# Optimization experiments

Measured on AMD Instinct MI355X. Metric: run time of the kernel, lower is better.

## Reference

```python
import jax, jax.numpy as jnp
import numpy as np

D = 1024
K = 3  # depthwise conv kernel size, causal (left pad K-1)


def setup_inputs() -> dict:
    key = jax.random.key(0)
    ks = jax.random.split(key, 6)
    B, L = 16, 2048
    x = jax.random.normal(ks[0], (B, L, D), dtype=jnp.float32)
    s_in = 1.0 / np.sqrt(D)
    Win = jax.random.uniform(ks[1], (3 * D, D), minval=-s_in, maxval=s_in, dtype=jnp.float32)
    bin_ = jax.random.uniform(ks[2], (3 * D,), minval=-s_in, maxval=s_in, dtype=jnp.float32)
    # depthwise Conv1d weight (D, 1, K) -> stored as (D, K)
    s_c = 1.0 / np.sqrt(K)  # fan_in = in_channels/groups * K = K
    wconv = jax.random.uniform(ks[3], (D, K), minval=-s_c, maxval=s_c, dtype=jnp.float32)
    Wout = jax.random.uniform(ks[4], (D, D), minval=-s_in, maxval=s_in, dtype=jnp.float32)
    bout = jax.random.uniform(ks[5], (D,), minval=-s_in, maxval=s_in, dtype=jnp.float32)
    return {"x": x, "Win": Win, "bin_": bin_, "wconv": wconv, "Wout": Wout, "bout": bout}


def reference(x, Win, bin_, wconv, Wout, bout):
    # x: (B, L, D). in_proj -> (B, L, 3D); chunk along channel dim == last dim here
    BCx = jnp.einsum('bld,ed->ble', x, Win) + bin_
    Bg, Cg, xg = jnp.split(BCx, 3, axis=-1)  # each (B, L, D)
    Bx = Bg * xg
    L = Bx.shape[1]
    # causal depthwise conv: pad K-1 zeros on the left of time axis
    xp = jnp.pad(Bx, ((0, 0), (K - 1, 0), (0, 0)))
    conv_out = (wconv[:, 0] * xp[:, 0:L]
                + wconv[:, 1] * xp[:, 1:L + 1]
                + wconv[:, 2] * xp[:, 2:L + 2])  # (B, L, D)
    y = Cg * conv_out
    return jnp.einsum('bld,ed->ble', y, Wout) + bout
```

## Files before the change

### kernel.cpp

```cpp
#include <hip/hip_runtime.h>
#include <hip/hip_bf16.h>

#define D_    1024
#define LSEQ  2048
#define BATCH 16
#define M_    (BATCH * LSEQ)
#define K_    1024
#define N1    3072

typedef __bf16 bf16x8 __attribute__((ext_vector_type(8)));
typedef float  f32x4  __attribute__((ext_vector_type(4)));
typedef unsigned short us8 __attribute__((ext_vector_type(8)));

__device__ __forceinline__ unsigned short f2bf(float f) {
  unsigned u = __float_as_uint(f);
  u += 0x7FFFu + ((u >> 16) & 1u);
  return (unsigned short)(u >> 16);
}

__device__ __forceinline__ float bf2f(unsigned short h) {
  return __uint_as_float(((unsigned)h) << 16);
}

__global__ __launch_bounds__(256) void cvt_f32_bf16(const float* __restrict__ in,
                                                    unsigned short* __restrict__ out,
                                                    int n4) {
  int i = blockIdx.x * 256 + threadIdx.x;
  if (i < n4) {
    float4 v = ((const float4*)in)[i];
    ushort4 o;
    o.x = f2bf(v.x); o.y = f2bf(v.y); o.z = f2bf(v.z); o.w = f2bf(v.w);
    ((ushort4*)out)[i] = o;
  }
}

#define BM 128
#define BN 128
#define BK 32

__device__ __forceinline__ void gload_lds16(const void* g, void* l) {
  __builtin_amdgcn_global_load_lds((const __attribute__((address_space(1))) void*)g,
                                   (__attribute__((address_space(3))) void*)l,
                                   16, 0, 0);
}

template <int OUT_BF16>
__global__ __launch_bounds__(256) void gemm_bt(const unsigned short* __restrict__ A,
                                               const unsigned short* __restrict__ B,
                                               const float* __restrict__ bias,
                                               void* __restrict__ Cv,
                                               int M, int N, int K) {
  __shared__ unsigned short As[BM * BK];
  __shared__ unsigned short Bs[BN * BK];

  const int tid  = threadIdx.x;
  const int lane = tid & 63;
  const int wave = tid >> 6;
  const int quad = lane >> 4;
  const int l16  = lane & 15;
  const int wm   = wave & 1;
  const int wn   = wave >> 1;
  const int m0   = blockIdx.y * BM;
  const int n0   = blockIdx.x * BN;

  const int r0 = tid >> 2;
  const int s0 = (tid & 3) * 8;
  const unsigned short* a0 = A + (long)(m0 + r0) * K + s0;
  const unsigned short* a1 = a0 + (long)64 * K;
  const unsigned short* b0 = B + (long)(n0 + r0) * K + s0;
  const unsigned short* b1 = b0 + (long)64 * K;
  unsigned short* lA0 = &As[tid * 8];
  unsigned short* lA1 = &As[(256 + tid) * 8];
  unsigned short* lB0 = &Bs[tid * 8];
  unsigned short* lB1 = &Bs[(256 + tid) * 8];

  f32x4 acc[4][4] = {};

  for (int k0 = 0; k0 < K; k0 += BK) {
    gload_lds16(a0 + k0, lA0);
    gload_lds16(a1 + k0, lA1);
    gload_lds16(b0 + k0, lB0);
    gload_lds16(b1 + k0, lB1);
    __syncthreads();

    bf16x8 af[4], bfr[4];
#pragma unroll
    for (int mi = 0; mi < 4; ++mi)
      af[mi] = *(const bf16x8*)&As[(wm * 64 + mi * 16 + l16) * BK + quad * 8];
#pragma unroll
    for (int ni = 0; ni < 4; ++ni)
      bfr[ni] = *(const bf16x8*)&Bs[(wn * 64 + ni * 16 + l16) * BK + quad * 8];

#pragma unroll
    for (int mi = 0; mi < 4; ++mi)
#pragma unroll
      for (int ni = 0; ni < 4; ++ni)
        acc[mi][ni] = __builtin_amdgcn_mfma_f32_16x16x32_bf16(af[mi], bfr[ni],
                                                              acc[mi][ni], 0, 0, 0);
    __syncthreads();
  }

#pragma unroll
  for (int ni = 0; ni < 4; ++ni) {
    int col = n0 + wn * 64 + ni * 16 + l16;
    float bv = bias[col];
#pragma unroll
    for (int mi = 0; mi < 4; ++mi) {
      int row = m0 + wm * 64 + mi * 16 + quad * 4;
      f32x4 v = acc[mi][ni];
#pragma unroll
      for (int r = 0; r < 4; ++r) {
        float o = v[r] + bv;
        if (OUT_BF16)
          ((unsigned short*)Cv)[(long)(row + r) * N + col] = f2bf(o);
        else
          ((float*)Cv)[(long)(row + r) * N + col] = o;
      }
    }
  }
}

__global__ __launch_bounds__(256) void conv_mul(const unsigned short* __restrict__ BCx,
                                                const float* __restrict__ wconv,
                                                unsigned short* __restrict__ y) {
  __shared__ float wt[3][D_];
  for (int i = threadIdx.x; i < D_; i += 256) {
    wt[0][i] = wconv[i * 3 + 0];
    wt[1][i] = wconv[i * 3 + 1];
    wt[2][i] = wconv[i * 3 + 2];
  }
  __syncthreads();

  int idx = blockIdx.x * 256 + threadIdx.x;
  int bl  = idx >> 7;
  int d8  = (idx & 127) * 8;
  int l   = bl & (LSEQ - 1);
  const unsigned short* row = BCx + (long)bl * N1;

  us8 bg0 = *(const us8*)&row[d8];
  us8 xg0 = *(const us8*)&row[2048 + d8];
  us8 cg  = *(const us8*)&row[1024 + d8];

  float bx0[8], bx1[8], bx2[8];
#pragma unroll
  for (int j = 0; j < 8; ++j) { bx0[j] = bf2f(bg0[j]) * bf2f(xg0[j]); bx1[j] = 0.f; bx2[j] = 0.f; }

  if (l >= 1) {
    us8 bg1 = *(const us8*)&row[-N1 + d8];
    us8 xg1 = *(const us8*)&row[-N1 + 2048 + d8];
#pragma unroll
    for (int j = 0; j < 8; ++j) bx1[j] = bf2f(bg1[j]) * bf2f(xg1[j]);
  }
  if (l >= 2) {
    us8 bg2 = *(const us8*)&row[-2 * N1 + d8];
    us8 xg2 = *(const us8*)&row[-2 * N1 + 2048 + d8];
#pragma unroll
    for (int j = 0; j < 8; ++j) bx2[j] = bf2f(bg2[j]) * bf2f(xg2[j]);
  }

  us8 outv;
#pragma unroll
  for (int j = 0; j < 8; ++j) {
    float conv = wt[0][d8 + j] * bx2[j] + wt[1][d8 + j] * bx1[j] + wt[2][d8 + j] * bx0[j];
    outv[j] = f2bf(bf2f(cg[j]) * conv);
  }
  *(us8*)&y[(long)bl * D_ + d8] = outv;
}

extern "C" void kernel_launch(void* const* d_in, const int* in_sizes, int n_in,
                              void* d_out, int out_size, void* d_ws, size_t ws_size,
                              hipStream_t stream) {
  const float* x     = (const float*)d_in[0];
  const float* Win   = (const float*)d_in[1];
  const float* bin   = (const float*)d_in[2];
  const float* wconv = (const float*)d_in[3];
  const float* Wout  = (const float*)d_in[4];
  const float* bout  = (const float*)d_in[5];

  char* ws = (char*)d_ws;
  unsigned short* x_b    = (unsigned short*)(ws);
  unsigned short* Win_b  = (unsigned short*)(ws + 67108864);
  unsigned short* Wout_b = (unsigned short*)(ws + 73400320);
  unsigned short* BCx_b  = (unsigned short*)(ws + 75497472);
  unsigned short* y_b    = (unsigned short*)(ws + 276824064);

  cvt_f32_bf16<<<(M_ * K_ / 4) / 256, 256, 0, stream>>>(x, x_b, M_ * K_ / 4);
  cvt_f32_bf16<<<(N1 * K_ / 4) / 256, 256, 0, stream>>>(Win, Win_b, N1 * K_ / 4);
  cvt_f32_bf16<<<(D_ * K_ / 4) / 256, 256, 0, stream>>>(Wout, Wout_b, D_ * K_ / 4);

  {
    dim3 grid(N1 / BN, M_ / BM);
    gemm_bt<1><<<grid, 256, 0, stream>>>(x_b, Win_b, bin, BCx_b, M_, N1, K_);
  }

  conv_mul<<<(M_ * (D_ / 8)) / 256, 256, 0, stream>>>(BCx_b, wconv, y_b);

  {
    dim3 grid(D_ / BN, M_ / BM);
    gemm_bt<0><<<grid, 256, 0, stream>>>(y_b, Wout_b, bout, d_out, M_, D_, K_);
  }
}
```

Baseline: 668.1 us.

## Fuse gating and causal conv into GEMM epilogues, drop BCx intermediate

Splits the in-projection GEMM into two launches. The first computes the B and x gate columns together and writes only their product Bx in bf16. The second computes the C gate columns and applies the causal depthwise conv over Bx plus the C multiply in its epilogue, which removes the standalone conv kernel and the 3D-wide BCx buffer. Epilogues now stage tiles through LDS for coalesced vector stores, at the cost of extra barriers and LDS reuse.

Measured after the change: 631.4 us. 5.5% less time.

```diff
diff --git a/kernel.cpp b/kernel.cpp
--- a/kernel.cpp
+++ b/kernel.cpp
@@ -3,21 +3,17 @@
 
 #define D_    1024
 #define LSEQ  2048
-#define BATCH 16
-#define M_    (BATCH * LSEQ)
+#define M_    32768
 #define K_    1024
-#define N1    3072
 
 typedef __bf16 bf16x8 __attribute__((ext_vector_type(8)));
 typedef float  f32x4  __attribute__((ext_vector_type(4)));
-typedef unsigned short us8 __attribute__((ext_vector_type(8)));
 
 __device__ __forceinline__ unsigned short f2bf(float f) {
   unsigned u = __float_as_uint(f);
   u += 0x7FFFu + ((u >> 16) & 1u);
   return (unsigned short)(u >> 16);
 }
-
 __device__ __forceinline__ float bf2f(unsigned short h) {
   return __uint_as_float(((unsigned)h) << 16);
 }
@@ -34,8 +30,6 @@
   }
 }
 
-#define BM 128
-#define BN 128
 #define BK 32
 
 __device__ __forceinline__ void gload_lds16(const void* g, void* l) {
@@ -44,14 +38,18 @@
                                    16, 0, 0);
 }
 
-template <int OUT_BF16>
-__global__ __launch_bounds__(256) void gemm_bt(const unsigned short* __restrict__ A,
-                                               const unsigned short* __restrict__ B,
-                                               const float* __restrict__ bias,
-                                               void* __restrict__ Cv,
-                                               int M, int N, int K) {
-  __shared__ unsigned short As[BM * BK];
-  __shared__ unsigned short Bs[BN * BK];
+template <int MODE>
+__global__ __launch_bounds__(256) void gemm_fused(const unsigned short* __restrict__ A,
+                                                  const unsigned short* __restrict__ Wb,
+                                                  const float* __restrict__ biasA,
+                                                  const float* __restrict__ biasB,
+                                                  const unsigned short* __restrict__ Bx,
+                                                  const float* __restrict__ wconv,
+                                                  void* __restrict__ Outv) {
+  __shared__ __align__(16) char smem[16896];
+  unsigned short* As = (unsigned short*)smem;
+  unsigned short* Bs = (unsigned short*)(smem + 8192);
+  float* tr = (float*)smem;
 
   const int tid  = threadIdx.x;
   const int lane = tid & 63;
@@ -60,15 +58,31 @@
   const int l16  = lane & 15;
   const int wm   = wave & 1;
   const int wn   = wave >> 1;
-  const int m0   = blockIdx.y * BM;
-  const int n0   = blockIdx.x * BN;
+  const int m0   = blockIdx.y * 128;
+
+  const unsigned short* B0p;
+  const unsigned short* B1p;
+  int n0;
+  if (MODE == 0) {
+    n0  = blockIdx.x * 64;
+    B0p = Wb + (long)n0 * K_;
+    B1p = Wb + (long)(2048 + n0) * K_;
+  } else if (MODE == 1) {
+    n0  = blockIdx.x * 128;
+    B0p = Wb + (long)(1024 + n0) * K_;
+    B1p = B0p + (long)64 * K_;
+  } else {
+    n0  = blockIdx.x * 128;
+    B0p = Wb + (long)n0 * K_;
+    B1p = B0p + (long)64 * K_;
+  }
 
   const int r0 = tid >> 2;
   const int s0 = (tid & 3) * 8;
-  const unsigned short* a0 = A + (long)(m0 + r0) * K + s0;
-  const unsigned short* a1 = a0 + (long)64 * K;
-  const unsigned short* b0 = B + (long)(n0 + r0) * K + s0;
-  const unsigned short* b1 = b0 + (long)64 * K;
+  const unsigned short* a0 = A + (long)(m0 + r0) * K_ + s0;
+  const unsigned short* a1 = a0 + (long)64 * K_;
+  const unsigned short* b0 = B0p + (long)r0 * K_ + s0;
+  const unsigned short* b1 = B1p + (long)r0 * K_ + s0;
   unsigned short* lA0 = &As[tid * 8];
   unsigned short* lA1 = &As[(256 + tid) * 8];
   unsigned short* lB0 = &Bs[tid * 8];
@@ -76,7 +90,7 @@
 
   f32x4 acc[4][4] = {};
 
-  for (int k0 = 0; k0 < K; k0 += BK) {
+  for (int k0 = 0; k0 < K_; k0 += BK) {
     gload_lds16(a0 + k0, lA0);
     gload_lds16(a1 + k0, lA1);
     gload_lds16(b0 + k0, lB0);
@@ -100,71 +114,81 @@
     __syncthreads();
   }
 
+  float bv[4];
 #pragma unroll
   for (int ni = 0; ni < 4; ++ni) {
-    int col = n0 + wn * 64 + ni * 16 + l16;
-    float bv = bias[col];
-#pragma unroll
-    for (int mi = 0; mi < 4; ++mi) {
-      int row = m0 + wm * 64 + mi * 16 + quad * 4;
+    int col = wn * 64 + ni * 16 + l16;
+    if (MODE == 0)
+      bv[ni] = (col < 64) ? biasA[n0 + col] : biasB[n0 + col - 64];
+    else
+      bv[ni] = biasA[n0 + col];
+  }
+
+  const int rr   = tid >> 3;
+  const int cgid = tid & 7;
+
+#pragma unroll
+  for (int mi = 0; mi < 4; ++mi) {
+#pragma unroll
+    for (int ni = 0; ni < 4; ++ni) {
+      int col = wn * 64 + ni * 16 + l16;
       f32x4 v = acc[mi][ni];
 #pragma unroll
-      for (int r = 0; r < 4; ++r) {
-        float o = v[r] + bv;
-        if (OUT_BF16)
-          ((unsigned short*)Cv)[(long)(row + r) * N + col] = f2bf(o);
-        else
-          ((float*)Cv)[(long)(row + r) * N + col] = o;
+      for (int r = 0; r < 4; ++r)
+        tr[(wm * 16 + quad * 4 + r) * 132 + col] = v[r] + bv[ni];
+    }
+    __syncthreads();
+
+    int grow = m0 + (rr >> 4) * 64 + mi * 16 + (rr & 15);
+
+    if (MODE == 0) {
+      unsigned short* Out = (unsigned short*)Outv;
+#pragma unroll
+      for (int j = 0; j < 2; ++j) {
+        int c = (cgid + j * 8) * 4;
+        f32x4 bg = *(const f32x4*)&tr[rr * 132 + c];
+        f32x4 xg = *(const f32x4*)&tr[rr * 132 + 64 + c];
+        ushort4 o;
+        o.x = f2bf(bg[0] * xg[0]); o.y = f2bf(bg[1] * xg[1]);
+        o.z = f2bf(bg[2] * xg[2]); o.w = f2bf(bg[3] * xg[3]);
+        *(ushort4*)&Out[(long)grow * D_ + n0 + c] = o;
+      }
+    } else if (MODE == 1) {
+      unsigned short* Y = (unsigned short*)Outv;
+      int l = grow & (LSEQ - 1);
+#pragma unroll
+      for (int j = 0; j < 4; ++j) {
+        int c = (cgid + j * 8) * 4;
+        int d = n0 + c;
+        f32x4 cg = *(const f32x4*)&tr[rr * 132 + c];
+        f32x4 w0 = *(const f32x4*)&wconv[d * 3];
+        f32x4 w1 = *(const f32x4*)&wconv[d * 3 + 4];
+        f32x4 w2 = *(const f32x4*)&wconv[d * 3 + 8];
+        float wk0[4] = {w0[0], w0[3], w1[2], w2[1]};
+        float wk1[4] = {w0[1], w1[0], w1[3], w2[2]};
+        float wk2[4] = {w0[2], w1[1], w2[0], w2[3]};
+        ushort4 zz = {0, 0, 0, 0};
+        ushort4 x0 = *(const ushort4*)&Bx[(long)grow * D_ + d];
+        ushort4 x1 = (l >= 1) ? *(const ushort4*)&Bx[(long)(grow - 1) * D_ + d] : zz;
+        ushort4 x2 = (l >= 2) ? *(const ushort4*)&Bx[(long)(grow - 2) * D_ + d] : zz;
+        ushort4 o;
+        o.x = f2bf(cg[0] * (wk0[0] * bf2f(x2.x) + wk1[0] * bf2f(x1.x) + wk2[0] * bf2f(x0.x)));
+        o.y = f2bf(cg[1] * (wk0[1] * bf2f(x2.y) + wk1[1] * bf2f(x1.y) + wk2[1] * bf2f(x0.y)));
+        o.z = f2bf(cg[2] * (wk0[2] * bf2f(x2.z) + wk1[2] * bf2f(x1.z) + wk2[2] * bf2f(x0.z)));
+        o.w = f2bf(cg[3] * (wk0[3] * bf2f(x2.w) + wk1[3] * bf2f(x1.w) + wk2[3] * bf2f(x0.w)));
+        *(ushort4*)&Y[(long)grow * D_ + d] = o;
+      }
+    } else {
+      float* Out = (float*)Outv;
+#pragma unroll
+      for (int j = 0; j < 4; ++j) {
+        int c = (cgid + j * 8) * 4;
+        f32x4 v = *(const f32x4*)&tr[rr * 132 + c];
+        *(f32x4*)&Out[(long)grow * D_ + n0 + c] = v;
       }
     }
-  }
-}
-
-__global__ __launch_bounds__(256) void conv_mul(const unsigned short* __restrict__ BCx,
-                                                const float* __restrict__ wconv,
-                                                unsigned short* __restrict__ y) {
-  __shared__ float wt[3][D_];
-  for (int i = threadIdx.x; i < D_; i += 256) {
-    wt[0][i] = wconv[i * 3 + 0];
-    wt[1][i] = wconv[i * 3 + 1];
-    wt[2][i] = wconv[i * 3 + 2];
-  }
-  __syncthreads();
-
-  int idx = blockIdx.x * 256 + threadIdx.x;
-  int bl  = idx >> 7;
-  int d8  = (idx & 127) * 8;
-  int l   = bl & (LSEQ - 1);
-  const unsigned short* row = BCx + (long)bl * N1;
-
-  us8 bg0 = *(const us8*)&row[d8];
-  us8 xg0 = *(const us8*)&row[2048 + d8];
-  us8 cg  = *(const us8*)&row[1024 + d8];
-
-  float bx0[8], bx1[8], bx2[8];
-#pragma unroll
-  for (int j = 0; j < 8; ++j) { bx0[j] = bf2f(bg0[j]) * bf2f(xg0[j]); bx1[j] = 0.f; bx2[j] = 0.f; }
-
-  if (l >= 1) {
-    us8 bg1 = *(const us8*)&row[-N1 + d8];
-    us8 xg1 = *(const us8*)&row[-N1 + 2048 + d8];
-#pragma unroll
-    for (int j = 0; j < 8; ++j) bx1[j] = bf2f(bg1[j]) * bf2f(xg1[j]);
-  }
-  if (l >= 2) {
-    us8 bg2 = *(const us8*)&row[-2 * N1 + d8];
-    us8 xg2 = *(const us8*)&row[-2 * N1 + 2048 + d8];
-#pragma unroll
-    for (int j = 0; j < 8; ++j) bx2[j] = bf2f(bg2[j]) * bf2f(xg2[j]);
-  }
-
-  us8 outv;
-#pragma unroll
-  for (int j = 0; j < 8; ++j) {
-    float conv = wt[0][d8 + j] * bx2[j] + wt[1][d8 + j] * bx1[j] + wt[2][d8 + j] * bx0[j];
-    outv[j] = f2bf(bf2f(cg[j]) * conv);
-  }
-  *(us8*)&y[(long)bl * D_ + d8] = outv;
+    __syncthreads();
+  }
 }
 
 extern "C" void kernel_launch(void* const* d_in, const int* in_sizes, int n_in,
@@ -181,22 +205,26 @@
   unsigned short* x_b    = (unsigned short*)(ws);
   unsigned short* Win_b  = (unsigned short*)(ws + 67108864);
   unsigned short* Wout_b = (unsigned short*)(ws + 73400320);
-  unsigned short* BCx_b  = (unsigned short*)(ws + 75497472);
-  unsigned short* y_b    = (unsigned short*)(ws + 276824064);
+  unsigned short* Bx_b   = (unsigned short*)(ws + 75497472);
+  unsigned short* y_b    = (unsigned short*)(ws + 142606336);
 
   cvt_f32_bf16<<<(M_ * K_ / 4) / 256, 256, 0, stream>>>(x, x_b, M_ * K_ / 4);
-  cvt_f32_bf16<<<(N1 * K_ / 4) / 256, 256, 0, stream>>>(Win, Win_b, N1 * K_ / 4);
+  cvt_f32_bf16<<<(3072 * K_ / 4) / 256, 256, 0, stream>>>(Win, Win_b, 3072 * K_ / 4);
   cvt_f32_bf16<<<(D_ * K_ / 4) / 256, 256, 0, stream>>>(Wout, Wout_b, D_ * K_ / 4);
 
   {
-    dim3 grid(N1 / BN, M_ / BM);
-    gemm_bt<1><<<grid, 256, 0, stream>>>(x_b, Win_b, bin, BCx_b, M_, N1, K_);
-  }
-
-  conv_mul<<<(M_ * (D_ / 8)) / 256, 256, 0, stream>>>(BCx_b, wconv, y_b);
-
+    dim3 grid(D_ / 64, M_ / 128);
+    gemm_fused<0><<<grid, 256, 0, stream>>>(x_b, Win_b, bin, bin + 2048,
+                                            nullptr, nullptr, Bx_b);
+  }
   {
-    dim3 grid(D_ / BN, M_ / BM);
-    gemm_bt<0><<<grid, 256, 0, stream>>>(y_b, Wout_b, bout, d_out, M_, D_, K_);
-  }
-}
+    dim3 grid(D_ / 128, M_ / 128);
+    gemm_fused<1><<<grid, 256, 0, stream>>>(x_b, Win_b, bin + 1024, nullptr,
+                                            Bx_b, wconv, y_b);
+  }
+  {
+    dim3 grid(D_ / 128, M_ / 128);
+    gemm_fused<2><<<grid, 256, 0, stream>>>(y_b, Wout_b, bout, nullptr,
+                                            nullptr, nullptr, d_out);
+  }
+}
```
